# Optimization experiments

Measured on AMD Instinct MI355X. Metric: run time of the kernel, lower is better.

Reference implementation:

```python
import jax, jax.numpy as jnp
import numpy as np

B, C, H, W = 4, 128, 128, 128
NCLS = 80
NCONV = 2


def conv3x3(x, w, b):
    # x: [B,Cin,H,W], w: [Cout,Cin,3,3]
    y = jax.lax.conv_general_dilated(x, w, (1, 1), 'SAME',
                                     dimension_numbers=('NCHW', 'OIHW', 'NCHW'))
    return y + b[None, :, None, None]


def setup_inputs() -> dict:
    key = jax.random.key(0)
    ks = jax.random.split(key, 10)
    std = 0.01  # conv init std in the torch module
    prior_prob = 0.01
    bias_value = -np.log((1 - prior_prob) / prior_prob)
    inp = {
        'feature': jax.random.normal(ks[0], (B, C, H, W), jnp.float32),
        'targets': jax.random.uniform(ks[1], (B, NCLS, H, W), jnp.float32),
        'cls_w': std * jax.random.normal(ks[2], (NCONV, C, C, 3, 3), jnp.float32),
        'cls_b': jnp.zeros((NCONV, C), jnp.float32),
        'bbox_w': std * jax.random.normal(ks[3], (NCONV, C, C, 3, 3), jnp.float32),
        'bbox_b': jnp.zeros((NCONV, C), jnp.float32),
        'off_w': std * jax.random.normal(ks[4], (NCONV, C, C, 3, 3), jnp.float32),
        'off_b': jnp.zeros((NCONV, C), jnp.float32),
        'cls_score_w': std * jax.random.normal(ks[5], (NCLS, C, 3, 3), jnp.float32),
        'cls_score_b': jnp.full((NCLS,), bias_value, jnp.float32),
        'bbox_pred_w': std * jax.random.normal(ks[6], (2, C, 3, 3), jnp.float32),
        'bbox_pred_b': jnp.zeros((2,), jnp.float32),
        'center_off_w': std * jax.random.normal(ks[7], (2, C, 3, 3), jnp.float32),
        'center_off_b': jnp.zeros((2,), jnp.float32),
        'K': 100,
    }
    return inp


def centernet_forward(feature, targets, cls_w, cls_b, bbox_w, bbox_b, off_w, off_b,
                      cls_score_w, cls_score_b, bbox_pred_w, bbox_pred_b,
                      center_off_w, center_off_b, K):
    # ---- head: three conv+ReLU subnets + final 3x3 heads ----
    xc, xb, xo = feature, feature, feature
    for i in range(NCONV):
        xc = jax.nn.relu(conv3x3(xc, cls_w[i], cls_b[i]))
        xb = jax.nn.relu(conv3x3(xb, bbox_w[i], bbox_b[i]))
        xo = jax.nn.relu(conv3x3(xo, off_w[i], off_b[i]))
    logits = conv3x3(xc, cls_score_w, cls_score_b)      # [B,NCLS,H,W]
    wh = conv3x3(xb, bbox_pred_w, bbox_pred_b)          # [B,2,H,W]
    off = conv3x3(xo, center_off_w, center_off_b)       # [B,2,H,W]

    # ---- center focal loss (alpha=2, beta=4, reduction='sum') ----
    pos = (targets == 1.0).astype(logits.dtype)
    neg = (targets < 1.0).astype(logits.dtype)
    neg_w = jnp.power(1.0 - targets, 4.0)
    p = jax.nn.sigmoid(logits)
    log_p = jax.nn.log_sigmoid(logits)        # log(sigmoid(x))
    log_1mp = jax.nn.log_sigmoid(-logits)     # log(1 - sigmoid(x))
    pos_loss = log_p * jnp.square(1.0 - p) * pos
    neg_loss = log_1mp * jnp.square(p) * neg_w * neg
    loss = -(pos_loss.sum()) - (neg_loss.sum())

    # ---- decode: sigmoid + 3x3 maxpool pseudo-NMS + top-k + gather ----
    hm = p  # sigmoid heatmap
    hmax = jax.lax.reduce_window(hm, -jnp.inf, jax.lax.max,
                                 (1, 1, 3, 3), (1, 1, 1, 1), 'SAME')
    hm_nms = jnp.where(hmax == hm, hm, 0.0)
    scores, inds = jax.lax.top_k(hm_nms.reshape(B, -1), K)  # [B,K]
    hw = H * W
    clses = inds // hw                 # [B,K] int class ids
    sp = inds % hw                     # spatial index
    ys = (sp // W).astype(jnp.float32)
    xs = (sp % W).astype(jnp.float32)
    # gather wh/offset at peak locations
    wh_k = jnp.take_along_axis(wh.reshape(B, 2, hw), sp[:, None, :], axis=2)    # [B,2,K]
    off_k = jnp.take_along_axis(off.reshape(B, 2, hw), sp[:, None, :], axis=2)  # [B,2,K]
    cx = xs + off_k[:, 0]
    cy = ys + off_k[:, 1]
    w_, h_ = wh_k[:, 0], wh_k[:, 1]
    boxes = jnp.stack([cx - w_ / 2, cy - h_ / 2, cx + w_ / 2, cy + h_ / 2], axis=-1)  # [B,K,4]
    return boxes, scores, clses, loss


def reference(feature, targets, cls_w, cls_b, bbox_w, bbox_b, off_w, off_b,
              cls_score_w, cls_score_b, bbox_pred_w, bbox_pred_b,
              center_off_w, center_off_b, K):
    return centernet_forward(feature, targets, cls_w, cls_b, bbox_w, bbox_b,
                             off_w, off_b, cls_score_w, cls_score_b,
                             bbox_pred_w, bbox_pred_b, center_off_w,
                             center_off_b, K)
```

## Files before the change

kernel.cpp:

```cpp
#include <hip/hip_runtime.h>
#include <hip/hip_bf16.h>
#include <math.h>

#define B_    4
#define C_    128
#define H_    128
#define W_    128
#define HW_   (H_*W_)
#define NCLS_ 80
#define KTOP  100
#define CAPB  2048

typedef __attribute__((ext_vector_type(8)))  short bf16x8;
typedef __attribute__((ext_vector_type(16))) float f32x16;

#define WSTG_B     16384
#define WIMG_B     589824
#define NIMG       7
#define XROWB      144
#define XCOLS      130
#define XPITCH     (XCOLS * XROWB)
#define XSZ        ((size_t)16 * 130 * XPITCH)
#define XLDS_B     25920
#define LDS_TOT    (2 * XLDS_B)
#define ZERO_N     20512

__device__ __forceinline__ unsigned bf16_rne(float x) {
    unsigned u = __float_as_uint(x);
    return (u + 0x7FFFu + ((u >> 16) & 1u)) >> 16;
}
__device__ __forceinline__ void split2(float v0, float v1, unsigned& hiP, unsigned& loP) {
    unsigned h0 = bf16_rne(v0), h1 = bf16_rne(v1);
    float r0 = v0 - __uint_as_float(h0 << 16);
    float r1 = v1 - __uint_as_float(h1 << 16);
    unsigned l0 = bf16_rne(r0), l1 = bf16_rne(r1);
    hiP = h0 | (h1 << 16);
    loP = l0 | (l1 << 16);
}

#define MFMA32(a, bvec, c) __builtin_amdgcn_mfma_f32_32x32x16_bf16(a, bvec, c, 0, 0, 0)

__global__ __launch_bounds__(256) void init_k(char* __restrict__ xa, char* __restrict__ xb,
                                              unsigned* __restrict__ sm, float* __restrict__ loss)
{
    const int i = blockIdx.x * 256 + threadIdx.x;
    if (i < 16512) {
        char* buf = (i < 8256) ? xa : xb;
        const int j = (i < 8256) ? i : i - 8256;
        int R, col;
        if (j < 4160) {
            const int g = j / 260, rr = j % 260;
            R = g * 130 + ((rr < 130) ? 0 : 129);
            col = rr % 130;
        } else {
            const int q = j - 4160;
            const int g = q / 256, m = q % 256;
            R = g * 130 + 1 + (m >> 1);
            col = (m & 1) ? 129 : 0;
        }
        char* p = buf + ((size_t)R * XCOLS + col) * XROWB;
        #pragma unroll
        for (int k = 0; k < 9; k++) *(uint4*)(p + k * 16) = make_uint4(0, 0, 0, 0);
    } else {
        const int k = i - 16512;
        if (k < ZERO_N) sm[k] = 0u;
        if (k == ZERO_N) *loss = 0.f;
    }
}

struct WtArgs { const float* src[NIMG]; int cout[NIMG]; };

__global__ __launch_bounds__(256) void wtx_k(WtArgs a, unsigned short* wt)
{
    const int img = blockIdx.z;
    const int idx = blockIdx.x * 256 + threadIdx.x;
    const int h  = idx & 1;
    const int ks = (idx >> 1) & 1;
    const int r  = (idx >> 2) & 31;
    const int g  = (idx >> 7) & 3;
    const int st = idx >> 9;
    if (st >= 36) return;
    const int tap = st % 9, chunk = st / 9;
    const float* w = a.src[img];
    const int Cout = a.cout[img];
    const int cout = g * 32 + r;
    const int cin0 = chunk * 32 + ks * 16 + h * 8;
    float v[8];
    #pragma unroll
    for (int j = 0; j < 8; j++)
        v[j] = (cout < Cout) ? w[((size_t)cout * 128 + cin0 + j) * 9 + tap] : 0.f;
    unsigned hiW[4], loW[4];
    #pragma unroll
    for (int j = 0; j < 4; j++) split2(v[2 * j], v[2 * j + 1], hiW[j], loW[j]);
    char* dst = (char*)wt + (size_t)img * WIMG_B + (size_t)st * WSTG_B
              + g * 4096 + ks * 2048 + r * 32 + h * 16;
    *(uint4*)dst          = make_uint4(hiW[0], hiW[1], hiW[2], hiW[3]);
    *(uint4*)(dst + 1024) = make_uint4(loW[0], loW[1], loW[2], loW[3]);
}

template<int RELU, int XOUT>
__device__ __forceinline__ void conv_epilogue(
    f32x16 (&acc)[2], bool act,
    const float* bias, float* outf, char* outx, int Cout,
    int b, int x0, int y0, int wm, int wn, int kh, int l31)
{
    if (!act) return;
    if (XOUT == 0) {
        #pragma unroll
        for (int r = 0; r < 16; r++) {
            const int co = wm * 32 + 4 * kh + (r & 3) + 8 * (r >> 2);
            if (co < Cout) {
                const float bv = bias[co];
                #pragma unroll
                for (int fn = 0; fn < 2; fn++) {
                    const int p = wn * 64 + fn * 32 + l31;
                    float v = acc[fn][r] + bv;
                    if (RELU) v = fmaxf(v, 0.f);
                    outf[((size_t)b * Cout + co) * HW_ + (size_t)(y0 + (p >> 4)) * 128 + (x0 + (p & 15))] = v;
                }
            }
        }
    } else {
        const int chunkO = wm;
        #pragma unroll
        for (int r2 = 0; r2 < 8; r2++) {
            const int r = 2 * r2;
            const int cij = 4 * kh + (r & 3) + 8 * (r >> 2);
            const int co0 = wm * 32 + cij;
            const float b0v = bias[co0], b1v = bias[co0 + 1];
            #pragma unroll
            for (int fn = 0; fn < 2; fn++) {
                const int p = wn * 64 + fn * 32 + l31;
                float v0 = acc[fn][r] + b0v;
                float v1 = acc[fn][r + 1] + b1v;
                if (RELU) { v0 = fmaxf(v0, 0.f); v1 = fmaxf(v1, 0.f); }
                unsigned hiP, loP; split2(v0, v1, hiP, loP);
                char* rowp = outx + ((size_t)((b * 4 + chunkO) * 130 + (y0 + (p >> 4) + 1)) * XCOLS
                                    + (x0 + (p & 15) + 1)) * XROWB;
                *(unsigned*)(rowp + 2 * cij)      = hiP;
                *(unsigned*)(rowp + 64 + 2 * cij) = loP;
            }
        }
    }
}

#define WLOAD_(SLOT, SIDX) do {                                               \
    const char* wp_ = wb + (size_t)(SIDX) * WSTG_B;                           \
    wf[SLOT][0] = *(const bf16x8*)(wp_);                                      \
    wf[SLOT][1] = *(const bf16x8*)(wp_ + 2048);                               \
    wf[SLOT][2] = *(const bf16x8*)(wp_ + 1024);                               \
    wf[SLOT][3] = *(const bf16x8*)(wp_ + 3072);                               \
} while (0)

#define MFMA_TAP_(CUR, DOFF) do {                                             \
    if (act) {                                                                \
        _Pragma("unroll")                                                     \
        for (int ks = 0; ks < 2; ks++) {                                      \
            bf16x8 bh[2], bl[2];                                              \
            _Pragma("unroll")                                                 \
            for (int fn = 0; fn < 2; fn++) {                                  \
                bh[fn] = *(const bf16x8*)(lds + baddr[fn] + (DOFF) + ks * 32);      \
                bl[fn] = *(const bf16x8*)(lds + baddr[fn] + (DOFF) + ks * 32 + 64); \
            }                                                                 \
            _Pragma("unroll")                                                 \
            for (int fn = 0; fn < 2; fn++)                                    \
                acc[fn] = MFMA32(wf[CUR][ks], bh[fn], acc[fn]);               \
            _Pragma("unroll")                                                 \
            for (int fn = 0; fn < 2; fn++)                                    \
                acc[fn] = MFMA32(wf[CUR][ks], bl[fn], acc[fn]);               \
            _Pragma("unroll")                                                 \
            for (int fn = 0; fn < 2; fn++)                                    \
                acc[fn] = MFMA32(wf[CUR][2 + ks], bh[fn], acc[fn]);           \
        }                                                                     \
    }                                                                         \
} while (0)

template<int RELU, int XOUT>
__global__ __launch_bounds__(512) void conv_f_k(
    const float* __restrict__ in, const unsigned short* __restrict__ wt,
    const float* __restrict__ bias, float* __restrict__ outf,
    char* __restrict__ outx, int Cout)
{
    __shared__ __align__(16) char lds[LDS_TOT];

    const int t    = threadIdx.x;
    const int lane = t & 63;
    const int wv   = t >> 6;
    const int wm   = wv >> 1;
    const int wn   = wv & 1;
    const int l31  = lane & 31;
    const int kh   = lane >> 5;

    const int bi = blockIdx.x;
    const int x0 = (bi & 7) << 4;
    const int y0 = ((bi >> 3) & 15) << 3;
    const int b  = bi >> 7;

    int baddr[2];
    #pragma unroll
    for (int fn = 0; fn < 2; fn++) {
        const int p = wn * 64 + fn * 32 + l31;
        baddr[fn] = ((p >> 4) * 18 + (p & 15)) * 144 + kh * 16;
    }
    const bool act = (wm * 32) < Cout;

    const int wlane = ((lane & 31) << 5) | (kh << 4);
    const char* wb = (const char*)wt + wm * 4096 + wlane;

    f32x16 acc[2];
    #pragma unroll
    for (int j = 0; j < 2; j++)
        #pragma unroll
        for (int r = 0; r < 16; r++) acc[j][r] = 0.f;

    const float* inb = in + (size_t)b * 128 * HW_;

    bf16x8 wf[2][4];
    if (act) WLOAD_(0, 0);

    float xa[6], xb[6];
    #define LOADX(ch) do {                                                    \
        _Pragma("unroll")                                                     \
        for (int it = 0; it < 6; it++) {                                      \
            const int idx = t + it * 512;                                     \
            const int pl = idx & 15, cp = (idx >> 4) & 15, ph = idx >> 8;     \
            const int pos = ph * 16 + pl;                                     \
            float v0 = 0.f, v1 = 0.f;                                         \
            if (pos < 180) {                                                  \
                const int hy = pos / 18, hx = pos - hy * 18;                  \
                const int gy = y0 - 1 + hy, gx = x0 - 1 + hx;                 \
                if ((unsigned)gy < 128u && (unsigned)gx < 128u) {             \
                    const float* p0 = inb + (size_t)((ch) * 32 + 2 * cp) * HW_ \
                                          + gy * 128 + gx;                    \
                    v0 = p0[0]; v1 = p0[HW_];                                 \
                }                                                             \
            }                                                                 \
            xa[it] = v0; xb[it] = v1;                                         \
        }                                                                     \
    } while (0)

    #define STOREX(bufsel) do {                                               \
        _Pragma("unroll")                                                     \
        for (int it = 0; it < 6; it++) {                                      \
            const int idx = t + it * 512;                                     \
            const int pl = idx & 15, cp = (idx >> 4) & 15, ph = idx >> 8;     \
            const int pos = ph * 16 + pl;                                     \
            if (pos < 180) {                                                  \
                unsigned hiP, loP; split2(xa[it], xb[it], hiP, loP);          \
                *(unsigned*)(lds + (bufsel) * XLDS_B + pos * 144 + 4 * cp)      = hiP; \
                *(unsigned*)(lds + (bufsel) * XLDS_B + pos * 144 + 64 + 4 * cp) = loP; \
            }                                                                 \
        }                                                                     \
    } while (0)

    LOADX(0);
    STOREX(0);
    __syncthreads();

    #define TAPF(CH, TAP, CUR, NXT) do {                                      \
        if (act && ((CH) * 9 + (TAP) + 1 < 36)) WLOAD_(NXT, (CH) * 9 + (TAP) + 1); \
        MFMA_TAP_(CUR, (((TAP) / 3) * 18 + ((TAP) % 3)) * 144 + ((CH) & 1) * XLDS_B); \
    } while (0)

    #define CHUNKF(CH, SA, SB) do {                                           \
        TAPF(CH, 0, SA, SB); TAPF(CH, 1, SB, SA); TAPF(CH, 2, SA, SB);        \
        TAPF(CH, 3, SB, SA); TAPF(CH, 4, SA, SB); TAPF(CH, 5, SB, SA);        \
        if ((CH) < 3) LOADX((CH) + 1);                                        \
        TAPF(CH, 6, SA, SB); TAPF(CH, 7, SB, SA); TAPF(CH, 8, SA, SB);        \
        if ((CH) < 3) { STOREX(((CH) + 1) & 1); __syncthreads(); }            \
    } while (0)

    CHUNKF(0, 0, 1);
    CHUNKF(1, 1, 0);
    CHUNKF(2, 0, 1);
    CHUNKF(3, 1, 0);

    #undef LOADX
    #undef STOREX
    #undef TAPF
    #undef CHUNKF
    conv_epilogue<RELU, XOUT>(acc, act, bias, outf, outx, Cout, b, x0, y0, wm, wn, kh, l31);
}

template<int RELU, int XOUT>
__global__ __launch_bounds__(512) void conv_x_k(
    const char* __restrict__ xin, const unsigned short* __restrict__ wt,
    const float* __restrict__ bias, float* __restrict__ outf,
    char* __restrict__ outx, int Cout)
{
    __shared__ __align__(16) char lds[LDS_TOT];

    const int t    = threadIdx.x;
    const int lane = t & 63;
    const int wv   = t >> 6;
    const int wm   = wv >> 1;
    const int wn   = wv & 1;
    const int l31  = lane & 31;
    const int kh   = lane >> 5;

    const int bi = blockIdx.x;
    const int x0 = (bi & 7) << 4;
    const int y0 = ((bi >> 3) & 15) << 3;
    const int b  = bi >> 7;

    int baddr[2];
    #pragma unroll
    for (int fn = 0; fn < 2; fn++) {
        const int p = wn * 64 + fn * 32 + l31;
        baddr[fn] = (p >> 4) * 2592 + (p & 15) * 144 + kh * 16;
    }
    const bool act = (wm * 32) < Cout;

    const int wlane = ((lane & 31) << 5) | (kh << 4);
    const char* wb = (const char*)wt + wm * 4096 + wlane;

    f32x16 acc[2];
    #pragma unroll
    for (int j = 0; j < 2; j++)
        #pragma unroll
        for (int r = 0; r < 16; r++) acc[j][r] = 0.f;

    bf16x8 wf[2][4];
    if (act) WLOAD_(0, 0);

    const int nst = (wv < 4) ? 3 : 2;
    const int st0 = (wv < 4) ? wv * 3 : 12 + (wv - 4) * 2;

    {
        const size_t rowbase = ((size_t)((b * 4 + 0) * 130 + y0) * XCOLS + x0) * XROWB;
        for (int gg = 0; gg < nst; gg++) {
            const int g = st0 + gg;
            const int hy = g >> 1, ii = g & 1;
            __builtin_amdgcn_global_load_lds(
                (const __attribute__((address_space(1))) unsigned*)
                    (xin + rowbase + (size_t)hy * XPITCH + ii * 1024 + lane * 16),
                (__attribute__((address_space(3))) unsigned*)(lds + hy * 2592 + ii * 1024),
                16, 0, 0);
        }
        if (t < 340) {
            const int hy = t / 34;
            const int off = 2048 + (t % 34) * 16;
            uint4 v = *(const uint4*)(xin + rowbase + (size_t)hy * XPITCH + off);
            *(uint4*)(lds + hy * 2592 + off) = v;
        }
    }
    __syncthreads();

    #define TAPX(CH, TAP, CUR, NXT) do {                                      \
        if (act && ((CH) * 9 + (TAP) + 1 < 36)) WLOAD_(NXT, (CH) * 9 + (TAP) + 1); \
        MFMA_TAP_(CUR, ((TAP) / 3) * 2592 + ((TAP) % 3) * 144 + ((CH) & 1) * XLDS_B); \
    } while (0)

    #define CHUNKX(CH, SA, SB) do {                                           \
        uint4 tl0_; bool h0_ = false;                                         \
        const int xd_ = (((CH) + 1) & 1) * XLDS_B;                            \
        if ((CH) < 3) {                                                       \
            const size_t rowb1_ = ((size_t)((b * 4 + (CH) + 1) * 130 + y0) * XCOLS + x0) * XROWB; \
            for (int gg = 0; gg < nst; gg++) {                                \
                const int g = st0 + gg;                                       \
                const int hy = g >> 1, ii = g & 1;                            \
                __builtin_amdgcn_global_load_lds(                             \
                    (const __attribute__((address_space(1))) unsigned*)       \
                        (xin + rowb1_ + (size_t)hy * XPITCH + ii * 1024 + lane * 16), \
                    (__attribute__((address_space(3))) unsigned*)(lds + xd_ + hy * 2592 + ii * 1024), \
                    16, 0, 0);                                                \
            }                                                                 \
            if (t < 340) {                                                    \
                const int hy = t / 34;                                        \
                const int off = 2048 + (t % 34) * 16;                         \
                tl0_ = *(const uint4*)(xin + rowb1_ + (size_t)hy * XPITCH + off); \
                h0_ = true;                                                   \
            }                                                                 \
        }                                                                     \
        TAPX(CH, 0, SA, SB); TAPX(CH, 1, SB, SA); TAPX(CH, 2, SA, SB);        \
        TAPX(CH, 3, SB, SA); TAPX(CH, 4, SA, SB); TAPX(CH, 5, SB, SA);        \
        TAPX(CH, 6, SA, SB); TAPX(CH, 7, SB, SA); TAPX(CH, 8, SA, SB);        \
        if ((CH) < 3) {                                                       \
            if (h0_) {                                                        \
                const int hy = t / 34;                                        \
                const int off = 2048 + (t % 34) * 16;                         \
                *(uint4*)(lds + xd_ + hy * 2592 + off) = tl0_;                \
            }                                                                 \
            __syncthreads();                                                  \
        }                                                                     \
    } while (0)

    CHUNKX(0, 0, 1);
    CHUNKX(1, 1, 0);
    CHUNKX(2, 0, 1);
    CHUNKX(3, 1, 0);

    #undef TAPX
    #undef CHUNKX
    conv_epilogue<RELU, XOUT>(acc, act, bias, outf, outx, Cout, b, x0, y0, wm, wn, kh, l31);
}

__global__ __launch_bounds__(256) void conv2out_k(
    const float* __restrict__ in, const float* __restrict__ w,
    const float* __restrict__ bias, float* __restrict__ out)
{
    __shared__ float ws[128 * 9 * 2];
    const int t = threadIdx.x;
    for (int i = t; i < 2304; i += 256) {
        const int co = i & 1, tap = (i >> 1) % 9, ci = i / 18;
        ws[i] = w[(size_t)co * 1152 + ci * 9 + tap];
    }
    __syncthreads();

    const int b  = blockIdx.y;
    const int y  = (blockIdx.x >> 3) * 16 + (t >> 4);
    const int x  = (blockIdx.x & 7) * 16 + (t & 15);
    const float* inb = in + (size_t)b * 128 * HW_ + y * 128 + x;

    float a0 = bias[0], a1 = bias[1];
    #pragma unroll 2
    for (int ci = 0; ci < 128; ci++) {
        const float* p  = inb + (size_t)ci * HW_;
        const float* wp = ws + ci * 18;
        #pragma unroll
        for (int tap = 0; tap < 9; tap++) {
            const int dy = tap / 3 - 1, dx = tap % 3 - 1;
            const int yy = y + dy, xx = x + dx;
            float v = 0.f;
            if ((unsigned)yy < 128u && (unsigned)xx < 128u) v = p[dy * 128 + dx];
            a0 = fmaf(v, wp[tap * 2 + 0], a0);
            a1 = fmaf(v, wp[tap * 2 + 1], a1);
        }
    }
    out[((size_t)b * 2 + 0) * HW_ + y * 128 + x] = a0;
    out[((size_t)b * 2 + 1) * HW_ + y * 128 + x] = a1;
}

__global__ __launch_bounds__(256) void lnh_k(
    const float* __restrict__ L, const float* __restrict__ targets,
    float* __restrict__ loss_out, unsigned* __restrict__ keys,
    unsigned* __restrict__ hist)
{
    __shared__ unsigned h[2048];
    for (int j = threadIdx.x; j < 2048; j += 256) h[j] = 0;
    __syncthreads();

    const int per_b = NCLS_ * HW_;
    const int b = blockIdx.y;
    const float* Lb = L + (size_t)b * per_b;
    const float* Tb = targets + (size_t)b * per_b;
    unsigned* kb = keys + (size_t)b * per_b;

    float sum = 0.f;
    for (int i = blockIdx.x * 256 + threadIdx.x; i < per_b; i += gridDim.x * 256) {
        const float x = Lb[i];
        const float t = Tb[i];
        const float e   = expf(-fabsf(x));
        const float inv = 1.f / (1.f + e);
        const float lp  = log1pf(e);
        const bool  xe  = (x >= 0.f);
        const float p   = xe ? inv : e * inv;
        const float lsp = xe ? -lp : (x - lp);
        const float lsn = lsp - x;
        float om = 1.f - t;
        float nw = om * om; nw *= nw;
        const float omp = 1.f - p;
        if (t == 1.0f)     sum -= lsp * omp * omp;
        else if (t < 1.0f) sum -= lsn * p * p * nw;

        const int sp = i & (HW_ - 1);
        const int y = sp >> 7, xq = sp & 127;
        const float* plane = Lb + (i - sp);
        const int ym = (y > 0) ? y - 1 : 0,   yp = (y < 127) ? y + 1 : 127;
        const int xm = (xq > 0) ? xq - 1 : 0, xp = (xq < 127) ? xq + 1 : 127;
        const float* r0 = plane + ym * 128;
        const float* r1 = plane + y  * 128;
        const float* r2 = plane + yp * 128;
        float m = fmaxf(fmaxf(fmaxf(r0[xm], r0[xq]), fmaxf(r0[xp], r1[xm])),
                 fmaxf(fmaxf(x, r1[xp]),
                 fmaxf(fmaxf(r2[xm], r2[xq]), r2[xp])));
        const float em   = expf(-fabsf(m));
        const float invm = 1.f / (1.f + em);
        const float pm   = (m >= 0.f) ? invm : em * invm;
        const unsigned key = (__float_as_uint(p) == __float_as_uint(pm)) ? __float_as_uint(p) : 0u;
        kb[i] = key;
        if (key) atomicAdd(&h[key >> 21], 1u);
    }

    #pragma unroll
    for (int off = 32; off > 0; off >>= 1) sum += __shfl_down(sum, off, 64);
    __shared__ float wsum[4];
    int lane = threadIdx.x & 63, wid = threadIdx.x >> 6;
    if (lane == 0) wsum[wid] = sum;
    __syncthreads();
    if (threadIdx.x == 0)
        atomicAdd(loss_out, wsum[0] + wsum[1] + wsum[2] + wsum[3]);

    unsigned* gh = hist + b * 2048;
    for (int j = threadIdx.x; j < 2048; j += 256) if (h[j]) atomicAdd(&gh[j], h[j]);
}

__global__ void hist2_k(const unsigned* __restrict__ keys, const unsigned* __restrict__ bin1,
                        unsigned* __restrict__ hist)
{
    __shared__ unsigned h[2048];
    for (int j = threadIdx.x; j < 2048; j += blockDim.x) h[j] = 0;
    __syncthreads();
    const int per_b = NCLS_ * HW_;
    const int b = blockIdx.y;
    const unsigned b1 = bin1[b];
    const unsigned* kb = keys + (size_t)b * per_b;
    for (int i = blockIdx.x * blockDim.x + threadIdx.x; i < per_b; i += gridDim.x * blockDim.x) {
        unsigned k = kb[i];
        if (k && (k >> 21) == b1) atomicAdd(&h[(k >> 10) & 2047], 1u);
    }
    __syncthreads();
    unsigned* gh = hist + b * 2048;
    for (int j = threadIdx.x; j < 2048; j += blockDim.x) if (h[j]) atomicAdd(&gh[j], h[j]);
}

__global__ void hist3_k(const unsigned* __restrict__ keys, const unsigned* __restrict__ pfx2,
                        unsigned* __restrict__ hist)
{
    __shared__ unsigned h[1024];
    for (int j = threadIdx.x; j < 1024; j += blockDim.x) h[j] = 0;
    __syncthreads();
    const int per_b = NCLS_ * HW_;
    const int b = blockIdx.y;
    const unsigned p2 = pfx2[b];
    const unsigned* kb = keys + (size_t)b * per_b;
    for (int i = blockIdx.x * blockDim.x + threadIdx.x; i < per_b; i += gridDim.x * blockDim.x) {
        unsigned k = kb[i];
        if (k && (k >> 10) == p2) atomicAdd(&h[k & 1023], 1u);
    }
    __syncthreads();
    unsigned* gh = hist + b * 1024;
    for (int j = threadIdx.x; j < 1024; j += blockDim.x) if (h[j]) atomicAdd(&gh[j], h[j]);
}

template<int NBINS, int LEVEL>
__global__ __launch_bounds__(256) void scan_k(
    const unsigned* __restrict__ hist,
    const unsigned* __restrict__ inPfx, const unsigned* __restrict__ inGt,
    unsigned* __restrict__ outPfx, unsigned* __restrict__ outGt)
{
    constexpr int PER = NBINS / 256;
    const int b = blockIdx.x;
    const int t = threadIdx.x;
    const unsigned* h = hist + b * NBINS;
    const unsigned base = (LEVEL == 1) ? 0u : inGt[b];

    unsigned v[PER];
    unsigned local = 0;
    #pragma unroll
    for (int i = 0; i < PER; i++) { v[i] = h[t * PER + i]; local += v[i]; }

    __shared__ unsigned ps[256];
    ps[t] = local;
    __syncthreads();
    #pragma unroll
    for (int off = 1; off < 256; off <<= 1) {
        unsigned add = (t + off < 256) ? ps[t + off] : 0u;
        __syncthreads();
        ps[t] += add;
        __syncthreads();
    }
    const unsigned sumAbove = (t == 255) ? 0u : ps[t + 1];

    unsigned sfx = sumAbove;
    #pragma unroll
    for (int i = PER - 1; i >= 0; i--) {
        unsigned sfx_next = sfx;
        sfx += v[i];
        bool cond     = (base + sfx      >= KTOP);
        bool condNext = (base + sfx_next >= KTOP);
        if (cond && !condNext) {
            unsigned sel = (unsigned)(t * PER + i);
            unsigned pfx = (LEVEL == 1) ? sel
                         : (LEVEL == 2) ? ((inPfx[b] << 11) | sel)
                                        : ((inPfx[b] << 10) | sel);
            outPfx[b] = pfx;
            outGt[b]  = base + sfx_next;
        }
    }
    if (t == 0 && base + ps[0] < KTOP) {
        unsigned pfx = (LEVEL == 1) ? 0u
                     : (LEVEL == 2) ? (inPfx[b] << 11)
                                    : (inPfx[b] << 10);
        outPfx[b] = pfx;
        outGt[b]  = base + ps[0];
    }
}

__global__ void select_k(const unsigned* __restrict__ keys, const unsigned* __restrict__ Tk,
                         unsigned* cntA, unsigned* cntB,
                         uint2* __restrict__ listA, unsigned* __restrict__ listB)
{
    const int per_b = NCLS_ * HW_;
    const int b = blockIdx.y;
    const unsigned T = Tk[b];
    const unsigned* kb = keys + (size_t)b * per_b;
    for (int i = blockIdx.x * blockDim.x + threadIdx.x; i < per_b; i += gridDim.x * blockDim.x) {
        unsigned k = kb[i];
        if (k > T) {
            unsigned pos = atomicAdd(&cntA[b], 1u);
            if (pos < KTOP) listA[b * KTOP + pos] = make_uint2(k, (unsigned)i);
        } else if (k == T && k != 0u) {
            unsigned pos = atomicAdd(&cntB[b], 1u);
            if (pos < CAPB) listB[b * CAPB + pos] = (unsigned)i;
        }
    }
}

__global__ void finalize_k(const unsigned* __restrict__ cntA, const unsigned* __restrict__ cntB,
                           const uint2* __restrict__ listA, const unsigned* __restrict__ listB,
                           const unsigned* __restrict__ Tk,
                           const float* __restrict__ wh, const float* __restrict__ off,
                           float* __restrict__ out)
{
    __shared__ unsigned sk[KTOP], si[KTOP], ok[KTOP], oi[KTOP];
    const int b = blockIdx.x;
    const int nA = (int)min(cntA[b], (unsigned)KTOP);
    const unsigned T = Tk[b];

    if ((int)threadIdx.x < nA) {
        uint2 e = listA[b * KTOP + threadIdx.x];
        sk[threadIdx.x] = e.x;
        si[threadIdx.x] = e.y;
    }
    __syncthreads();

    if (threadIdx.x == 0) {
        int need = KTOP - nA;
        unsigned nB = min(cntB[b], (unsigned)CAPB);
        long long prev = -1;
        for (int r = 0; r < need; r++) {
            unsigned best = 0xFFFFFFFFu;
            for (unsigned j = 0; j < nB; j++) {
                unsigned idx = listB[b * CAPB + j];
                if ((long long)idx > prev && idx < best) best = idx;
            }
            if (best == 0xFFFFFFFFu) { sk[nA + r] = 0u; si[nA + r] = 0u; }
            else { sk[nA + r] = T; si[nA + r] = best; prev = (long long)best; }
        }
    }
    __syncthreads();

    if (threadIdx.x < KTOP) {
        unsigned kk = sk[threadIdx.x], ii = si[threadIdx.x];
        int rank = 0;
        for (int j = 0; j < KTOP; j++) {
            unsigned kj = sk[j], ij = si[j];
            rank += (kj > kk) || (kj == kk && ij < ii);
        }
        ok[rank] = kk; oi[rank] = ii;
    }
    __syncthreads();

    if (threadIdx.x < KTOP) {
        int r = threadIdx.x;
        unsigned ind = oi[r];
        float score = __uint_as_float(ok[r]);
        int cls = (int)(ind / HW_);
        int sp  = (int)(ind % HW_);
        float ysf = (float)(sp >> 7);
        float xsf = (float)(sp & 127);
        float w0 = wh[((size_t)b * 2 + 0) * HW_ + sp];
        float h0 = wh[((size_t)b * 2 + 1) * HW_ + sp];
        float o0 = off[((size_t)b * 2 + 0) * HW_ + sp];
        float o1 = off[((size_t)b * 2 + 1) * HW_ + sp];
        float cx = xsf + o0;
        float cy = ysf + o1;
        float* boxes  = out;
        float* scores = out + (size_t)B_ * KTOP * 4;
        float* clses  = out + (size_t)B_ * KTOP * 5;
        boxes[((size_t)b * KTOP + r) * 4 + 0] = cx - w0 * 0.5f;
        boxes[((size_t)b * KTOP + r) * 4 + 1] = cy - h0 * 0.5f;
        boxes[((size_t)b * KTOP + r) * 4 + 2] = cx + w0 * 0.5f;
        boxes[((size_t)b * KTOP + r) * 4 + 3] = cy + h0 * 0.5f;
        scores[b * KTOP + r] = score;
        clses[b * KTOP + r]  = (float)cls;
    }
}

extern "C" void kernel_launch(void* const* d_in, const int* in_sizes, int n_in,
                              void* d_out, int out_size, void* d_ws, size_t ws_size,
                              hipStream_t stream)
{
    const float* feature      = (const float*)d_in[0];
    const float* targets      = (const float*)d_in[1];
    const float* cls_w        = (const float*)d_in[2];
    const float* cls_b        = (const float*)d_in[3];
    const float* bbox_w       = (const float*)d_in[4];
    const float* bbox_b       = (const float*)d_in[5];
    const float* off_w        = (const float*)d_in[6];
    const float* off_b        = (const float*)d_in[7];
    const float* cls_score_w  = (const float*)d_in[8];
    const float* cls_score_b  = (const float*)d_in[9];
    const float* bbox_pred_w  = (const float*)d_in[10];
    const float* bbox_pred_b  = (const float*)d_in[11];
    const float* center_off_w = (const float*)d_in[12];
    const float* center_off_b = (const float*)d_in[13];
    float* out = (float*)d_out;

    const size_t L_BYTES  = (size_t)B_ * NCLS_ * HW_ * 4;
    const size_t P_BYTES  = (size_t)B_ * 2 * HW_ * 4;
    const size_t WT_BYTES = (size_t)NIMG * WIMG_B;

    char* ws = (char*)d_ws;
    const size_t lw = (size_t)C_ * C_ * 9;
    float* loss_ptr = out + (size_t)B_ * KTOP * 6;

    char* XA = ws;
    char* XB = ws + XSZ;
    float* L   = (float*)(ws + 2 * XSZ);
    float* WH  = (float*)(ws + 2 * XSZ + L_BYTES);
    float* OFF = (float*)(ws + 2 * XSZ + L_BYTES + P_BYTES);
    unsigned short* WT = (unsigned short*)(ws + 2 * XSZ + L_BYTES + 2 * P_BYTES);
    unsigned* sm = (unsigned*)(ws + 2 * XSZ + L_BYTES + 2 * P_BYTES + WT_BYTES);
    float* Bf = (float*)XB;
    unsigned* keys = (unsigned*)XB;

    unsigned* hist1 = sm;
    unsigned* hist2 = sm + 4 * 2048;
    unsigned* hist3 = sm + 8 * 2048;
    unsigned* bin1  = sm + 8 * 2048 + 4 * 1024;
    unsigned* gt1   = bin1 + 4;
    unsigned* pfx2  = bin1 + 8;
    unsigned* gt2   = bin1 + 12;
    unsigned* Tk    = bin1 + 16;
    unsigned* gt3   = bin1 + 20;
    unsigned* cntA  = bin1 + 24;
    unsigned* cntB  = bin1 + 28;
    uint2*    listA = (uint2*)(bin1 + 32);
    unsigned* listB = (unsigned*)(bin1 + 32 + 2 * B_ * KTOP);

    WtArgs wa;
    wa.src[0] = cls_w;        wa.cout[0] = 128;
    wa.src[1] = bbox_w;       wa.cout[1] = 128;
    wa.src[2] = off_w;        wa.cout[2] = 128;
    wa.src[3] = cls_w + lw;   wa.cout[3] = 128;
    wa.src[4] = bbox_w + lw;  wa.cout[4] = 128;
    wa.src[5] = off_w + lw;   wa.cout[5] = 128;
    wa.src[6] = cls_score_w;  wa.cout[6] = NCLS_;

    init_k<<<145, 256, 0, stream>>>(XA, XB, sm, loss_ptr);
    wtx_k<<<dim3(72, 1, NIMG), 256, 0, stream>>>(wa, WT);

    #define WIMG(i) (WT + (size_t)(i) * (WIMG_B / 2))

    conv_f_k<1, 1><<<512, 512, 0, stream>>>(feature, WIMG(0), cls_b,       nullptr, XA, 128);
    conv_x_k<1, 1><<<512, 512, 0, stream>>>(XA,      WIMG(3), cls_b + C_,  nullptr, XB, 128);
    conv_x_k<0, 0><<<512, 512, 0, stream>>>(XB,      WIMG(6), cls_score_b, L, nullptr, NCLS_);
    conv_f_k<1, 1><<<512, 512, 0, stream>>>(feature, WIMG(1), bbox_b,      nullptr, XA, 128);
    conv_x_k<1, 0><<<512, 512, 0, stream>>>(XA,      WIMG(4), bbox_b + C_, Bf, nullptr, 128);
    conv2out_k<<<dim3(64, 4), 256, 0, stream>>>(Bf, bbox_pred_w, bbox_pred_b, WH);
    conv_f_k<1, 1><<<512, 512, 0, stream>>>(feature, WIMG(2), off_b,       nullptr, XA, 128);
    conv_x_k<1, 0><<<512, 512, 0, stream>>>(XA,      WIMG(5), off_b + C_,  Bf, nullptr, 128);
    conv2out_k<<<dim3(64, 4), 256, 0, stream>>>(Bf, center_off_w, center_off_b, OFF);

    lnh_k<<<dim3(512, B_), 256, 0, stream>>>(L, targets, loss_ptr, keys, hist1);

    dim3 hgrid(512, B_);
    scan_k<2048, 1><<<B_, 256, 0, stream>>>(hist1, nullptr, nullptr, bin1, gt1);
    hist2_k<<<hgrid, 256, 0, stream>>>(keys, bin1, hist2);
    scan_k<2048, 2><<<B_, 256, 0, stream>>>(hist2, bin1, gt1, pfx2, gt2);
    hist3_k<<<hgrid, 256, 0, stream>>>(keys, pfx2, hist3);
    scan_k<1024, 3><<<B_, 256, 0, stream>>>(hist3, pfx2, gt2, Tk, gt3);
    select_k<<<hgrid, 256, 0, stream>>>(keys, Tk, cntA, cntB, listA, listB);

    finalize_k<<<B_, 128, 0, stream>>>(cntA, cntB, listA, listB, Tk, WH, OFF, out);
}
```

Before: 676.1 us.

## Remap conv warps so each wave covers all output-channel groups for one pixel strip

The conv kernels drop from 8 waves (4 channel groups x 2 pixel halves) to 4 waves per block. Each wave now computes all four 32-channel output groups for 32 pixels, so one LDS activation fragment feeds four MFMAs instead of each wave re-reading it. LDS read traffic per MFMA falls, but each wave now holds four accumulators and 32 weight fragments, which raises register pressure and may limit occupancy. Launch bounds are set to 256 threads with 2 blocks per CU, and the staging loops are adjusted for the smaller block.

```diff
diff --git a/kernel.cpp b/kernel.cpp
--- a/kernel.cpp
+++ b/kernel.cpp
@@ -100,42 +100,35 @@
 
 template<int RELU, int XOUT>
 __device__ __forceinline__ void conv_epilogue(
-    f32x16 (&acc)[2], bool act,
+    f32x16 (&acc)[4], const bool* act,
     const float* bias, float* outf, char* outx, int Cout,
-    int b, int x0, int y0, int wm, int wn, int kh, int l31)
-{
-    if (!act) return;
-    if (XOUT == 0) {
-        #pragma unroll
-        for (int r = 0; r < 16; r++) {
-            const int co = wm * 32 + 4 * kh + (r & 3) + 8 * (r >> 2);
-            if (co < Cout) {
-                const float bv = bias[co];
-                #pragma unroll
-                for (int fn = 0; fn < 2; fn++) {
-                    const int p = wn * 64 + fn * 32 + l31;
-                    float v = acc[fn][r] + bv;
+    int b, int x0, int y0, int wv, int kh, int l31)
+{
+    const int p = wv * 32 + l31;
+    #pragma unroll
+    for (int g = 0; g < 4; g++) {
+        if (!act[g]) continue;
+        if (XOUT == 0) {
+            #pragma unroll
+            for (int r = 0; r < 16; r++) {
+                const int co = g * 32 + 4 * kh + (r & 3) + 8 * (r >> 2);
+                if (co < Cout) {
+                    float v = acc[g][r] + bias[co];
                     if (RELU) v = fmaxf(v, 0.f);
                     outf[((size_t)b * Cout + co) * HW_ + (size_t)(y0 + (p >> 4)) * 128 + (x0 + (p & 15))] = v;
                 }
             }
-        }
-    } else {
-        const int chunkO = wm;
-        #pragma unroll
-        for (int r2 = 0; r2 < 8; r2++) {
-            const int r = 2 * r2;
-            const int cij = 4 * kh + (r & 3) + 8 * (r >> 2);
-            const int co0 = wm * 32 + cij;
-            const float b0v = bias[co0], b1v = bias[co0 + 1];
+        } else {
             #pragma unroll
-            for (int fn = 0; fn < 2; fn++) {
-                const int p = wn * 64 + fn * 32 + l31;
-                float v0 = acc[fn][r] + b0v;
-                float v1 = acc[fn][r + 1] + b1v;
+            for (int r2 = 0; r2 < 8; r2++) {
+                const int r = 2 * r2;
+                const int cij = 4 * kh + (r & 3) + 8 * (r >> 2);
+                const int co0 = g * 32 + cij;
+                float v0 = acc[g][r] + bias[co0];
+                float v1 = acc[g][r + 1] + bias[co0 + 1];
                 if (RELU) { v0 = fmaxf(v0, 0.f); v1 = fmaxf(v1, 0.f); }
                 unsigned hiP, loP; split2(v0, v1, hiP, loP);
-                char* rowp = outx + ((size_t)((b * 4 + chunkO) * 130 + (y0 + (p >> 4) + 1)) * XCOLS
+                char* rowp = outx + ((size_t)((b * 4 + g) * 130 + (y0 + (p >> 4) + 1)) * XCOLS
                                     + (x0 + (p & 15) + 1)) * XROWB;
                 *(unsigned*)(rowp + 2 * cij)      = hiP;
                 *(unsigned*)(rowp + 64 + 2 * cij) = loP;
@@ -146,37 +139,34 @@
 
 #define WLOAD_(SLOT, SIDX) do {                                               \
     const char* wp_ = wb + (size_t)(SIDX) * WSTG_B;                           \
-    wf[SLOT][0] = *(const bf16x8*)(wp_);                                      \
-    wf[SLOT][1] = *(const bf16x8*)(wp_ + 2048);                               \
-    wf[SLOT][2] = *(const bf16x8*)(wp_ + 1024);                               \
-    wf[SLOT][3] = *(const bf16x8*)(wp_ + 3072);                               \
-} while (0)
-
-#define MFMA_TAP_(CUR, DOFF) do {                                             \
-    if (act) {                                                                \
-        _Pragma("unroll")                                                     \
-        for (int ks = 0; ks < 2; ks++) {                                      \
-            bf16x8 bh[2], bl[2];                                              \
-            _Pragma("unroll")                                                 \
-            for (int fn = 0; fn < 2; fn++) {                                  \
-                bh[fn] = *(const bf16x8*)(lds + baddr[fn] + (DOFF) + ks * 32);      \
-                bl[fn] = *(const bf16x8*)(lds + baddr[fn] + (DOFF) + ks * 32 + 64); \
-            }                                                                 \
-            _Pragma("unroll")                                                 \
-            for (int fn = 0; fn < 2; fn++)                                    \
-                acc[fn] = MFMA32(wf[CUR][ks], bh[fn], acc[fn]);               \
-            _Pragma("unroll")                                                 \
-            for (int fn = 0; fn < 2; fn++)                                    \
-                acc[fn] = MFMA32(wf[CUR][ks], bl[fn], acc[fn]);               \
-            _Pragma("unroll")                                                 \
-            for (int fn = 0; fn < 2; fn++)                                    \
-                acc[fn] = MFMA32(wf[CUR][2 + ks], bh[fn], acc[fn]);           \
-        }                                                                     \
+    _Pragma("unroll")                                                         \
+    for (int g_ = 0; g_ < 4; g_++) if (act[g_]) {                             \
+        wf[SLOT][g_ * 4 + 0] = *(const bf16x8*)(wp_ + g_ * 4096);             \
+        wf[SLOT][g_ * 4 + 1] = *(const bf16x8*)(wp_ + g_ * 4096 + 2048);      \
+        wf[SLOT][g_ * 4 + 2] = *(const bf16x8*)(wp_ + g_ * 4096 + 1024);      \
+        wf[SLOT][g_ * 4 + 3] = *(const bf16x8*)(wp_ + g_ * 4096 + 3072);      \
     }                                                                         \
 } while (0)
 
+#define MFMA_TAP_(CUR, DOFF) do {                                             \
+    _Pragma("unroll")                                                         \
+    for (int ks = 0; ks < 2; ks++) {                                          \
+        bf16x8 bh = *(const bf16x8*)(lds + baddr + (DOFF) + ks * 32);         \
+        bf16x8 bl = *(const bf16x8*)(lds + baddr + (DOFF) + ks * 32 + 64);    \
+        _Pragma("unroll")                                                     \
+        for (int g = 0; g < 4; g++) if (act[g])                               \
+            acc[g] = MFMA32(wf[CUR][g * 4 + ks], bh, acc[g]);                 \
+        _Pragma("unroll")                                                     \
+        for (int g = 0; g < 4; g++) if (act[g])                               \
+            acc[g] = MFMA32(wf[CUR][g * 4 + ks], bl, acc[g]);                 \
+        _Pragma("unroll")                                                     \
+        for (int g = 0; g < 4; g++) if (act[g])                               \
+            acc[g] = MFMA32(wf[CUR][g * 4 + 2 + ks], bh, acc[g]);             \
+    }                                                                         \
+} while (0)
+
 template<int RELU, int XOUT>
-__global__ __launch_bounds__(512) void conv_f_k(
+__global__ __launch_bounds__(256, 2) void conv_f_k(
     const float* __restrict__ in, const unsigned short* __restrict__ wt,
     const float* __restrict__ bias, float* __restrict__ outf,
     char* __restrict__ outx, int Cout)
@@ -186,8 +176,6 @@
     const int t    = threadIdx.x;
     const int lane = t & 63;
     const int wv   = t >> 6;
-    const int wm   = wv >> 1;
-    const int wn   = wv & 1;
     const int l31  = lane & 31;
     const int kh   = lane >> 5;
 
@@ -196,33 +184,32 @@
     const int y0 = ((bi >> 3) & 15) << 3;
     const int b  = bi >> 7;
 
-    int baddr[2];
-    #pragma unroll
-    for (int fn = 0; fn < 2; fn++) {
-        const int p = wn * 64 + fn * 32 + l31;
-        baddr[fn] = ((p >> 4) * 18 + (p & 15)) * 144 + kh * 16;
-    }
-    const bool act = (wm * 32) < Cout;
-
-    const int wlane = ((lane & 31) << 5) | (kh << 4);
-    const char* wb = (const char*)wt + wm * 4096 + wlane;
-
-    f32x16 acc[2];
-    #pragma unroll
-    for (int j = 0; j < 2; j++)
+    const int p0 = wv * 32 + l31;
+    const int baddr = ((p0 >> 4) * 18 + (p0 & 15)) * 144 + kh * 16;
+
+    bool act[4];
+    #pragma unroll
+    for (int g = 0; g < 4; g++) act[g] = (g * 32) < Cout;
+
+    const int wlane = (l31 << 5) | (kh << 4);
+    const char* wb = (const char*)wt + wlane;
+
+    f32x16 acc[4];
+    #pragma unroll
+    for (int g = 0; g < 4; g++)
         #pragma unroll
-        for (int r = 0; r < 16; r++) acc[j][r] = 0.f;
+        for (int r = 0; r < 16; r++) acc[g][r] = 0.f;
 
     const float* inb = in + (size_t)b * 128 * HW_;
 
-    bf16x8 wf[2][4];
-    if (act) WLOAD_(0, 0);
-
-    float xa[6], xb[6];
+    bf16x8 wf[2][16];
+    WLOAD_(0, 0);
+
+    float xa[12], xb[12];
     #define LOADX(ch) do {                                                    \
         _Pragma("unroll")                                                     \
-        for (int it = 0; it < 6; it++) {                                      \
-            const int idx = t + it * 512;                                     \
+        for (int it = 0; it < 12; it++) {                                     \
+            const int idx = t + it * 256;                                     \
             const int pl = idx & 15, cp = (idx >> 4) & 15, ph = idx >> 8;     \
             const int pos = ph * 16 + pl;                                     \
             float v0 = 0.f, v1 = 0.f;                                         \
@@ -230,9 +217,9 @@
                 const int hy = pos / 18, hx = pos - hy * 18;                  \
                 const int gy = y0 - 1 + hy, gx = x0 - 1 + hx;                 \
                 if ((unsigned)gy < 128u && (unsigned)gx < 128u) {             \
-                    const float* p0 = inb + (size_t)((ch) * 32 + 2 * cp) * HW_ \
+                    const float* pp = inb + (size_t)((ch) * 32 + 2 * cp) * HW_ \
                                           + gy * 128 + gx;                    \
-                    v0 = p0[0]; v1 = p0[HW_];                                 \
+                    v0 = pp[0]; v1 = pp[HW_];                                 \
                 }                                                             \
             }                                                                 \
             xa[it] = v0; xb[it] = v1;                                         \
@@ -241,8 +228,8 @@
 
     #define STOREX(bufsel) do {                                               \
         _Pragma("unroll")                                                     \
-        for (int it = 0; it < 6; it++) {                                      \
-            const int idx = t + it * 512;                                     \
+        for (int it = 0; it < 12; it++) {                                     \
+            const int idx = t + it * 256;                                     \
             const int pl = idx & 15, cp = (idx >> 4) & 15, ph = idx >> 8;     \
             const int pos = ph * 16 + pl;                                     \
             if (pos < 180) {                                                  \
@@ -258,7 +245,7 @@
     __syncthreads();
 
     #define TAPF(CH, TAP, CUR, NXT) do {                                      \
-        if (act && ((CH) * 9 + (TAP) + 1 < 36)) WLOAD_(NXT, (CH) * 9 + (TAP) + 1); \
+        if ((CH) * 9 + (TAP) + 1 < 36) WLOAD_(NXT, (CH) * 9 + (TAP) + 1);     \
         MFMA_TAP_(CUR, (((TAP) / 3) * 18 + ((TAP) % 3)) * 144 + ((CH) & 1) * XLDS_B); \
     } while (0)
 
@@ -279,11 +266,11 @@
     #undef STOREX
     #undef TAPF
     #undef CHUNKF
-    conv_epilogue<RELU, XOUT>(acc, act, bias, outf, outx, Cout, b, x0, y0, wm, wn, kh, l31);
+    conv_epilogue<RELU, XOUT>(acc, act, bias, outf, outx, Cout, b, x0, y0, wv, kh, l31);
 }
 
 template<int RELU, int XOUT>
-__global__ __launch_bounds__(512) void conv_x_k(
+__global__ __launch_bounds__(256, 2) void conv_x_k(
     const char* __restrict__ xin, const unsigned short* __restrict__ wt,
     const float* __restrict__ bias, float* __restrict__ outf,
     char* __restrict__ outx, int Cout)
@@ -293,8 +280,6 @@
     const int t    = threadIdx.x;
     const int lane = t & 63;
     const int wv   = t >> 6;
-    const int wm   = wv >> 1;
-    const int wn   = wv & 1;
     const int l31  = lane & 31;
     const int kh   = lane >> 5;
 
@@ -303,33 +288,30 @@
     const int y0 = ((bi >> 3) & 15) << 3;
     const int b  = bi >> 7;
 
-    int baddr[2];
-    #pragma unroll
-    for (int fn = 0; fn < 2; fn++) {
-        const int p = wn * 64 + fn * 32 + l31;
-        baddr[fn] = (p >> 4) * 2592 + (p & 15) * 144 + kh * 16;
-    }
-    const bool act = (wm * 32) < Cout;
-
-    const int wlane = ((lane & 31) << 5) | (kh << 4);
-    const char* wb = (const char*)wt + wm * 4096 + wlane;
-
-    f32x16 acc[2];
-    #pragma unroll
-    for (int j = 0; j < 2; j++)
+    const int p0 = wv * 32 + l31;
+    const int baddr = (p0 >> 4) * 2592 + (p0 & 15) * 144 + kh * 16;
+
+    bool act[4];
+    #pragma unroll
+    for (int g = 0; g < 4; g++) act[g] = (g * 32) < Cout;
+
+    const int wlane = (l31 << 5) | (kh << 4);
+    const char* wb = (const char*)wt + wlane;
+
+    f32x16 acc[4];
+    #pragma unroll
+    for (int g = 0; g < 4; g++)
         #pragma unroll
-        for (int r = 0; r < 16; r++) acc[j][r] = 0.f;
-
-    bf16x8 wf[2][4];
-    if (act) WLOAD_(0, 0);
-
-    const int nst = (wv < 4) ? 3 : 2;
-    const int st0 = (wv < 4) ? wv * 3 : 12 + (wv - 4) * 2;
+        for (int r = 0; r < 16; r++) acc[g][r] = 0.f;
+
+    bf16x8 wf[2][16];
+    WLOAD_(0, 0);
 
     {
         const size_t rowbase = ((size_t)((b * 4 + 0) * 130 + y0) * XCOLS + x0) * XROWB;
-        for (int gg = 0; gg < nst; gg++) {
-            const int g = st0 + gg;
+        #pragma unroll
+        for (int gg = 0; gg < 5; gg++) {
+            const int g = wv * 5 + gg;
             const int hy = g >> 1, ii = g & 1;
             __builtin_amdgcn_global_load_lds(
                 (const __attribute__((address_space(1))) unsigned*)
@@ -337,9 +319,9 @@
                 (__attribute__((address_space(3))) unsigned*)(lds + hy * 2592 + ii * 1024),
                 16, 0, 0);
         }
-        if (t < 340) {
-            const int hy = t / 34;
-            const int off = 2048 + (t % 34) * 16;
+        for (int u = t; u < 340; u += 256) {
+            const int hy = u / 34;
+            const int off = 2048 + (u % 34) * 16;
             uint4 v = *(const uint4*)(xin + rowbase + (size_t)hy * XPITCH + off);
             *(uint4*)(lds + hy * 2592 + off) = v;
         }
@@ -347,17 +329,18 @@
     __syncthreads();
 
     #define TAPX(CH, TAP, CUR, NXT) do {                                      \
-        if (act && ((CH) * 9 + (TAP) + 1 < 36)) WLOAD_(NXT, (CH) * 9 + (TAP) + 1); \
+        if ((CH) * 9 + (TAP) + 1 < 36) WLOAD_(NXT, (CH) * 9 + (TAP) + 1);     \
         MFMA_TAP_(CUR, ((TAP) / 3) * 2592 + ((TAP) % 3) * 144 + ((CH) & 1) * XLDS_B); \
     } while (0)
 
     #define CHUNKX(CH, SA, SB) do {                                           \
-        uint4 tl0_; bool h0_ = false;                                         \
+        uint4 tl0_, tl1_; bool h1_ = false;                                   \
         const int xd_ = (((CH) + 1) & 1) * XLDS_B;                            \
         if ((CH) < 3) {                                                       \
             const size_t rowb1_ = ((size_t)((b * 4 + (CH) + 1) * 130 + y0) * XCOLS + x0) * XROWB; \
-            for (int gg = 0; gg < nst; gg++) {                                \
-                const int g = st0 + gg;                                       \
+            _Pragma("unroll")                                                 \
+            for (int gg = 0; gg < 5; gg++) {                                  \
+                const int g = wv * 5 + gg;                                    \
                 const int hy = g >> 1, ii = g & 1;                            \
                 __builtin_amdgcn_global_load_lds(                             \
                     (const __attribute__((address_space(1))) unsigned*)       \
@@ -365,21 +348,29 @@
                     (__attribute__((address_space(3))) unsigned*)(lds + xd_ + hy * 2592 + ii * 1024), \
                     16, 0, 0);                                                \
             }                                                                 \
-            if (t < 340) {                                                    \
-                const int hy = t / 34;                                        \
-                const int off = 2048 + (t % 34) * 16;                         \
+            {                                                                 \
+                const int hy = t / 34, off = 2048 + (t % 34) * 16;            \
                 tl0_ = *(const uint4*)(xin + rowb1_ + (size_t)hy * XPITCH + off); \
-                h0_ = true;                                                   \
+            }                                                                 \
+            h1_ = (t < 84);                                                   \
+            if (h1_) {                                                        \
+                const int u = t + 256;                                        \
+                const int hy = u / 34, off = 2048 + (u % 34) * 16;            \
+                tl1_ = *(const uint4*)(xin + rowb1_ + (size_t)hy * XPITCH + off); \
             }                                                                 \
         }                                                                     \
         TAPX(CH, 0, SA, SB); TAPX(CH, 1, SB, SA); TAPX(CH, 2, SA, SB);        \
         TAPX(CH, 3, SB, SA); TAPX(CH, 4, SA, SB); TAPX(CH, 5, SB, SA);        \
         TAPX(CH, 6, SA, SB); TAPX(CH, 7, SB, SA); TAPX(CH, 8, SA, SB);        \
         if ((CH) < 3) {                                                       \
-            if (h0_) {                                                        \
-                const int hy = t / 34;                                        \
-                const int off = 2048 + (t % 34) * 16;                         \
+            {                                                                 \
+                const int hy = t / 34, off = 2048 + (t % 34) * 16;            \
                 *(uint4*)(lds + xd_ + hy * 2592 + off) = tl0_;                \
+            }                                                                 \
+            if (h1_) {                                                        \
+                const int u = t + 256;                                        \
+                const int hy = u / 34, off = 2048 + (u % 34) * 16;            \
+                *(uint4*)(lds + xd_ + hy * 2592 + off) = tl1_;                \
             }                                                                 \
             __syncthreads();                                                  \
         }                                                                     \
@@ -392,7 +383,7 @@
 
     #undef TAPX
     #undef CHUNKX
-    conv_epilogue<RELU, XOUT>(acc, act, bias, outf, outx, Cout, b, x0, y0, wm, wn, kh, l31);
+    conv_epilogue<RELU, XOUT>(acc, act, bias, outf, outx, Cout, b, x0, y0, wv, kh, l31);
 }
 
 __global__ __launch_bounds__(256) void conv2out_k(
@@ -744,14 +735,14 @@
 
     #define WIMG(i) (WT + (size_t)(i) * (WIMG_B / 2))
 
-    conv_f_k<1, 1><<<512, 512, 0, stream>>>(feature, WIMG(0), cls_b,       nullptr, XA, 128);
-    conv_x_k<1, 1><<<512, 512, 0, stream>>>(XA,      WIMG(3), cls_b + C_,  nullptr, XB, 128);
-    conv_x_k<0, 0><<<512, 512, 0, stream>>>(XB,      WIMG(6), cls_score_b, L, nullptr, NCLS_);
-    conv_f_k<1, 1><<<512, 512, 0, stream>>>(feature, WIMG(1), bbox_b,      nullptr, XA, 128);
-    conv_x_k<1, 0><<<512, 512, 0, stream>>>(XA,      WIMG(4), bbox_b + C_, Bf, nullptr, 128);
+    conv_f_k<1, 1><<<512, 256, 0, stream>>>(feature, WIMG(0), cls_b,       nullptr, XA, 128);
+    conv_x_k<1, 1><<<512, 256, 0, stream>>>(XA,      WIMG(3), cls_b + C_,  nullptr, XB, 128);
+    conv_x_k<0, 0><<<512, 256, 0, stream>>>(XB,      WIMG(6), cls_score_b, L, nullptr, NCLS_);
+    conv_f_k<1, 1><<<512, 256, 0, stream>>>(feature, WIMG(1), bbox_b,      nullptr, XA, 128);
+    conv_x_k<1, 0><<<512, 256, 0, stream>>>(XA,      WIMG(4), bbox_b + C_, Bf, nullptr, 128);
     conv2out_k<<<dim3(64, 4), 256, 0, stream>>>(Bf, bbox_pred_w, bbox_pred_b, WH);
-    conv_f_k<1, 1><<<512, 512, 0, stream>>>(feature, WIMG(2), off_b,       nullptr, XA, 128);
-    conv_x_k<1, 0><<<512, 512, 0, stream>>>(XA,      WIMG(5), off_b + C_,  Bf, nullptr, 128);
+    conv_f_k<1, 1><<<512, 256, 0, stream>>>(feature, WIMG(2), off_b,       nullptr, XA, 128);
+    conv_x_k<1, 0><<<512, 256, 0, stream>>>(XA,      WIMG(5), off_b + C_,  Bf, nullptr, 128);
     conv2out_k<<<dim3(64, 4), 256, 0, stream>>>(Bf, center_off_w, center_off_b, OFF);
 
     lnh_k<<<dim3(512, B_), 256, 0, stream>>>(L, targets, loss_ptr, keys, hist1);
```

Result: slower. 718.2 us (+6.2%).
